# Performance work log

Measured on AMD Instinct MI355X. Metric: run time of the kernel, lower is better.

The kernel has to match this reference:

```python
import jax, jax.numpy as jnp
import numpy as np

NUM_EXPERTS = 8
AUX_LOSS_COEF = 0.01


def setup_inputs() -> dict:
    key = jax.random.key(0)
    ks = jax.random.split(key, 5)
    B, S, D, E, H = 4, 2048, 1024, NUM_EXPERTS, 4096
    scale = 0.02  # typical init scale so gelu/softmax stay in sane ranges
    return {
        "hidden_states": jax.random.normal(ks[0], (B, S, D), dtype=jnp.float32),
        "router_w": jax.random.normal(ks[1], (D, E), dtype=jnp.float32) * scale,
        "router_b": jnp.zeros((E,), dtype=jnp.float32),
        "w1": jax.random.normal(ks[2], (E, D, H), dtype=jnp.float32) * scale,
        "b1": jnp.zeros((E, H), dtype=jnp.float32),
        "w2": jax.random.normal(ks[3], (E, H, D), dtype=jnp.float32) * scale,
        "b2": jnp.zeros((E, D), dtype=jnp.float32),
    }


def reference(hidden_states, router_w, router_b, w1, b1, w2, b2):
    B, S, D = hidden_states.shape
    E = w1.shape[0]
    x = hidden_states.reshape(-1, D)  # [T, D] flattened tokens

    # Switch router: top-1 expert, combine weight = softmax prob of chosen expert
    logits = x @ router_w + router_b                      # [T, E]
    probs = jax.nn.softmax(logits, axis=-1)               # [T, E]
    sel = jnp.argmax(logits, axis=-1)                     # [T] int
    gate = jnp.take_along_axis(probs, sel[:, None], axis=1)[:, 0]  # [T]

    # Expert FFNs: per-expert Linear -> gelu -> Linear, masked top-1 combine.
    # Loop is over the small fixed expert count (structurally distinct weights).
    out = jnp.zeros_like(x)
    for e in range(E):
        h = jax.nn.gelu(x @ w1[e] + b1[e])                # [T, H]
        ye = h @ w2[e] + b2[e]                            # [T, D]
        mask = (sel == e).astype(x.dtype)
        out = out + (mask * gate)[:, None] * ye

    # Switch load-balancing auxiliary loss
    mean_probs = probs.mean(axis=0)                       # [E]
    assignments = jnp.mean(jax.nn.one_hot(sel, E, dtype=x.dtype), axis=0)  # [E]
    aux_loss = jnp.sum(mean_probs * assignments) * E
    total_loss = AUX_LOSS_COEF * aux_loss

    return out.reshape(B, S, D), total_loss
```

## Files before the change

### kernel.cpp

```cpp
#include <hip/hip_runtime.h>
#include <cstdint>

typedef __bf16 bf16_t;
typedef __attribute__((ext_vector_type(8))) __bf16 bf16x8;
typedef __attribute__((ext_vector_type(4))) float f32x4;
typedef unsigned short ushort_t;

#define TOKENS 8192
#define DIM 1024
#define HID 4096
#define NEXP 8


__device__ __forceinline__ void gl_lds16(const void* g, void* l) {
  __builtin_amdgcn_global_load_lds(
      (__attribute__((address_space(1))) void*)(void*)g,
      (__attribute__((address_space(3))) void*)l, 16, 0, 0);
}

__device__ __forceinline__ float gelu_fast(float x) {
  float x2 = x * x;
  float z2 = x * (1.59576912f + 0.07135482f * x2);
  float e = __expf(-z2);
  return x * __builtin_amdgcn_rcpf(1.f + e);
}

template <int N>
__device__ __forceinline__ void pwait() {
  __builtin_amdgcn_sched_barrier(0);
  if constexpr (N == 8) asm volatile("s_waitcnt vmcnt(8)" ::: "memory");
  else if constexpr (N == 4) asm volatile("s_waitcnt vmcnt(4)" ::: "memory");
  else asm volatile("s_waitcnt vmcnt(0)" ::: "memory");
  __builtin_amdgcn_sched_barrier(0);
  __builtin_amdgcn_s_barrier();
  __builtin_amdgcn_sched_barrier(0);
}

__device__ __forceinline__ int xcd_chunk(int f, int nwg) {
  int q = nwg >> 3, r = nwg & 7;
  int xcd = f & 7, pos = f >> 3;
  return (xcd < r) ? (xcd * (q + 1) + pos) : (r * (q + 1) + (xcd - r) * q + pos);
}

__global__ void prep_kernel(const float* __restrict__ w1, bf16_t* __restrict__ w1t,
                            const float* __restrict__ x, const float* __restrict__ rw,
                            const float* __restrict__ rbias, bf16_t* __restrict__ xb,
                            int* __restrict__ sel, float* __restrict__ gate,
                            float* __restrict__ pprob, int* __restrict__ pcnt) {
  int bid = blockIdx.x;
  int t = threadIdx.x;
  if (bid < 8192) {
    __shared__ float tile[64][65];
    int e = bid >> 10, xb_ = bid & 1023;
    const float* src = w1 + (size_t)e * DIM * HID;
    bf16_t* dst = w1t + (size_t)e * DIM * HID;
    int rt = xb_ >> 6, ct = xb_ & 63;
    int rb = rt * 64, cb = ct * 64;
    int r = t >> 2, cq = (t & 3) * 16;
    const float* sp = src + (size_t)(rb + r) * HID + cb + cq;
#pragma unroll
    for (int j = 0; j < 16; j += 4) {
      float4 v = *(const float4*)(sp + j);
      tile[r][cq + j + 0] = v.x; tile[r][cq + j + 1] = v.y;
      tile[r][cq + j + 2] = v.z; tile[r][cq + j + 3] = v.w;
    }
    __syncthreads();
    int oc = t >> 2, orr = (t & 3) * 16;
    ushort_t tmp[16];
#pragma unroll
    for (int j = 0; j < 16; ++j) {
      bf16_t b = (bf16_t)tile[orr + j][oc];
      tmp[j] = __builtin_bit_cast(ushort_t, b);
    }
    uint4* dp = (uint4*)(dst + (size_t)(cb + oc) * DIM + rb + orr);
    dp[0] = ((uint4*)tmp)[0];
    dp[1] = ((uint4*)tmp)[1];
  } else {
    __shared__ float sprob[NEXP];
    __shared__ int scnt[NEXP];
    int rblk = bid - 8192;
    int lane = t & 63, wave = t >> 6;
    if (t < NEXP) { sprob[t] = 0.f; scnt[t] = 0; }
    __syncthreads();
    int tok = rblk * 4 + wave;
    const float* xp = x + (size_t)tok * DIM + lane * 16;
    float acc[NEXP];
#pragma unroll
    for (int e = 0; e < NEXP; ++e) acc[e] = 0.f;
    ushort_t xv[16];
#pragma unroll
    for (int j = 0; j < 16; j += 4) {
      float4 v = *(const float4*)(xp + j);
      const float* wr = rw + (size_t)(lane * 16 + j) * NEXP;
      float c[4] = {v.x, v.y, v.z, v.w};
#pragma unroll
      for (int d = 0; d < 4; ++d) {
        xv[j + d] = __builtin_bit_cast(ushort_t, (bf16_t)c[d]);
#pragma unroll
        for (int e = 0; e < NEXP; ++e) acc[e] += c[d] * wr[d * NEXP + e];
      }
    }
    {
      uint4* xop = (uint4*)(xb + (size_t)tok * DIM + lane * 16);
      xop[0] = ((uint4*)xv)[0];
      xop[1] = ((uint4*)xv)[1];
    }
#pragma unroll
    for (int s = 1; s < 64; s <<= 1)
#pragma unroll
      for (int e = 0; e < NEXP; ++e) acc[e] += __shfl_xor(acc[e], s);
    if (lane == 0) {
      float lg[NEXP];
#pragma unroll
      for (int e = 0; e < NEXP; ++e) lg[e] = acc[e] + rbias[e];
      float mx = lg[0]; int am = 0;
#pragma unroll
      for (int e = 1; e < NEXP; ++e) if (lg[e] > mx) { mx = lg[e]; am = e; }
      float p[NEXP]; float se = 0.f;
#pragma unroll
      for (int e = 0; e < NEXP; ++e) { p[e] = __expf(lg[e] - mx); se += p[e]; }
      float inv = 1.f / se;
#pragma unroll
      for (int e = 0; e < NEXP; ++e) { p[e] *= inv; atomicAdd(&sprob[e], p[e]); }
      sel[tok] = am;
      gate[tok] = p[am];
      atomicAdd(&scnt[am], 1);
    }
    __syncthreads();
    if (t < NEXP) {
      pprob[rblk * NEXP + t] = sprob[t];
      pcnt[rblk * NEXP + t] = scnt[t];
    }
  }
}

__global__ void reduce_kernel(const float* __restrict__ pprob, const int* __restrict__ pcnt,
                              int nb, int* __restrict__ meta, float* __restrict__ loss_out) {
  __shared__ float fred[256];
  __shared__ int ired[256];
  int t = threadIdx.x;
  int e = t & 7, i0 = t >> 3;
  float fs = 0.f; int is = 0;
  for (int i = i0; i < nb; i += 32) { fs += pprob[i * 8 + e]; is += pcnt[i * 8 + e]; }
  fred[t] = fs; ired[t] = is;
  __syncthreads();
  if (t < NEXP) {
    float tp = 0.f; int tc = 0;
    for (int j = 0; j < 32; ++j) { tp += fred[j * 8 + t]; tc += ired[j * 8 + t]; }
    meta[t] = tc;
    fred[t] = tp;
    meta[16 + t] = 0;
  }
  __syncthreads();
  if (t == 0) {
    int off = 0; float loss = 0.f; int s1 = 0, s2 = 0;
    for (int q = 0; q < NEXP; ++q) {
      int c = meta[q];
      meta[8 + q] = off;
      int nt1 = (c + 255) >> 8;
      for (int m = 0; m < nt1; ++m) meta[32 + s1++] = (q << 16) | m;
      int nt2 = (c + 127) >> 7;
      for (int m = 0; m < nt2; ++m) meta[96 + s2++] = (q << 16) | m;
      off += c;
      loss += (fred[q] / (float)TOKENS) * ((float)c / (float)TOKENS);
    }
    meta[24] = s1;
    meta[25] = s2;
    *loss_out = loss * (float)NEXP * 0.01f;
  }
}

__global__ void scatter_kernel(const int* __restrict__ sel, int* __restrict__ meta,
                               int* __restrict__ idxl) {
  int tok = blockIdx.x * 256 + threadIdx.x;
  int lane = threadIdx.x & 63;
  int e = sel[tok];
  const int* offsets = meta + 8;
  int* cursors = meta + 16;
#pragma unroll
  for (int ex = 0; ex < NEXP; ++ex) {
    unsigned long long mask = __ballot(e == ex);
    if (e == ex) {
      int leader = __ffsll(mask) - 1;
      int total = __popcll(mask);
      int rank = __popcll(mask & ((1ull << lane) - 1ull));
      int base = 0;
      if (lane == leader) base = atomicAdd(&cursors[ex], total);
      base = __shfl(base, leader);
      idxl[offsets[ex] + base + rank] = tok;
    }
  }
}

#define STG(Q, KT) do {                                                      \
    int _kb = (KT) * 32;                                                     \
    gl_lds16(apA0 + _kb, L + (Q) * 16384 + wave * 512);                      \
    gl_lds16(apA1 + _kb, L + (Q) * 16384 + 4096 + wave * 512);               \
    gl_lds16(bpB0 + _kb, L + (Q) * 16384 + 8192 + wave * 512);               \
    gl_lds16(bpB1 + _kb, L + (Q) * 16384 + 12288 + wave * 512);              \
  } while (0)

#define CMP(Q) do {                                                          \
    const bf16_t* Ab = L + (Q) * 16384;                                      \
    const bf16_t* Bb = Ab + 8192;                                            \
    bf16x8 bv[4];                                                            \
    _Pragma("unroll")                                                        \
    for (int n = 0; n < 4; ++n)                                              \
      bv[n] = *(const bf16x8*)&Bb[(wcol * 64 + n * 16 + l15) * 32 + ks];     \
    __builtin_amdgcn_s_setprio(1);                                           \
    _Pragma("unroll")                                                        \
    for (int m = 0; m < 8; ++m) {                                            \
      bf16x8 af = *(const bf16x8*)&Ab[(wrow * 128 + m * 16 + l15) * 32 + ks];\
      _Pragma("unroll")                                                      \
      for (int n = 0; n < 4; ++n)                                            \
        acc[m][n] = __builtin_amdgcn_mfma_f32_16x16x32_bf16(af, bv[n], acc[m][n], 0, 0, 0); \
    }                                                                        \
    __builtin_amdgcn_s_setprio(0);                                           \
  } while (0)

#define PIPE(NT) do {                                                        \
    STG(0, 0); STG(1, 1); STG(2, 2);                                         \
    pwait<8>();                                                              \
    _Pragma("unroll 1")                                                      \
    for (int kt = 0; kt < (NT) - 4; kt += 4) {                               \
      STG(3, kt + 3); CMP(0); pwait<8>();                                    \
      STG(0, kt + 4); CMP(1); pwait<8>();                                    \
      STG(1, kt + 5); CMP(2); pwait<8>();                                    \
      STG(2, kt + 6); CMP(3); pwait<8>();                                    \
    }                                                                        \
    STG(3, (NT) - 1); CMP(0); pwait<8>();                                    \
    CMP(1); pwait<4>();                                                      \
    CMP(2); pwait<0>();                                                      \
    CMP(3);                                                                  \
  } while (0)

#define G1_NWG 640
#define W2_NBLK 4096

__global__ __launch_bounds__(512, 2) void gemm1_kernel(
    const bf16_t* __restrict__ xb, const bf16_t* __restrict__ w1t,
    const float* __restrict__ b1, const int* __restrict__ idxl,
    const int* __restrict__ meta, bf16_t* __restrict__ h,
    const float* __restrict__ w2, bf16_t* __restrict__ w2t) {
  __shared__ __align__(16) char smemraw[131072];
  int f = blockIdx.x;
  int t = threadIdx.x;

  if (f >= G1_NWG) {
    float (*tile)[65] = (float(*)[65])smemraw;
    int tb = f - G1_NWG;
    int e = tb >> 9, xb_ = tb & 511;
    const float* src = w2 + (size_t)e * HID * DIM;
    bf16_t* dst = w2t + (size_t)e * HID * DIM;
    int rt = xb_ >> 4, ct = xb_ & 15;
    int rb = rt * 128, cb = ct * 64;
    int r = t >> 2, cq = (t & 3) * 16;
    const float* sp = src + (size_t)(rb + r) * DIM + cb + cq;
#pragma unroll
    for (int j = 0; j < 16; j += 4) {
      float4 v = *(const float4*)(sp + j);
      tile[r][cq + j + 0] = v.x; tile[r][cq + j + 1] = v.y;
      tile[r][cq + j + 2] = v.z; tile[r][cq + j + 3] = v.w;
    }
    __syncthreads();
    int oc = t >> 3, orr = (t & 7) * 16;
    ushort_t tmp[16];
#pragma unroll
    for (int j = 0; j < 16; ++j) {
      bf16_t b = (bf16_t)tile[orr + j][oc];
      tmp[j] = __builtin_bit_cast(ushort_t, b);
    }
    uint4* dp = (uint4*)(dst + (size_t)(cb + oc) * HID + rb + orr);
    dp[0] = ((uint4*)tmp)[0];
    dp[1] = ((uint4*)tmp)[1];
    return;
  }

  bf16_t* L = (bf16_t*)smemraw;
  int lf = xcd_chunk(f, G1_NWG);
  int slot = lf % 40, nt = lf / 40;
  if (slot >= meta[24]) return;
  int tm = meta[32 + slot];
  int e = tm >> 16, mt = tm & 0xffff;
  int cnt = meta[e];
  int off = meta[8 + e];
  int mBase = mt * 256;
  int nBase = nt * 256;
  int lane = t & 63, wave = t >> 6;
  int l15 = lane & 15, g = lane >> 4;
  int wrow = wave >> 2, wcol = wave & 3;
  int ks = (g ^ (l15 & 3)) * 8;
  f32x4 acc[8][4];
#pragma unroll
  for (int m = 0; m < 8; ++m)
#pragma unroll
    for (int n = 0; n < 4; ++n) acc[m][n] = (f32x4){0.f, 0.f, 0.f, 0.f};

  int srow = t >> 2;
  int koff = ((t & 3) ^ (srow & 3)) * 8;
  int c1 = cnt - 1;
  int sA0 = mBase + srow; sA0 = sA0 < c1 ? sA0 : c1;
  int sA1 = mBase + 128 + srow; sA1 = sA1 < c1 ? sA1 : c1;
  const bf16_t* apA0 = xb + (size_t)idxl[off + sA0] * DIM + koff;
  const bf16_t* apA1 = xb + (size_t)idxl[off + sA1] * DIM + koff;
  const bf16_t* wb = w1t + (size_t)e * HID * DIM;
  const bf16_t* bpB0 = wb + (size_t)(nBase + srow) * DIM + koff;
  const bf16_t* bpB1 = wb + (size_t)(nBase + 128 + srow) * DIM + koff;

  PIPE(32);

  float bias[4];
#pragma unroll
  for (int n = 0; n < 4; ++n) bias[n] = b1[e * HID + nBase + wcol * 64 + n * 16 + l15];
#pragma unroll
  for (int m = 0; m < 8; ++m) {
    int rb0 = mBase + wrow * 128 + m * 16 + g * 4;
#pragma unroll
    for (int j = 0; j < 4; ++j) {
      int r = rb0 + j;
      if (r < cnt) {
        bf16_t* hp = h + (size_t)(off + r) * HID + nBase + wcol * 64 + l15;
#pragma unroll
        for (int n = 0; n < 4; ++n)
          hp[n * 16] = (bf16_t)gelu_fast(acc[m][n][j] + bias[n]);
      }
    }
  }
}

__global__ __launch_bounds__(512, 2) void gemm2_kernel(
    const bf16_t* __restrict__ h, const bf16_t* __restrict__ w2t,
    const float* __restrict__ b2, const int* __restrict__ idxl,
    const float* __restrict__ gate, const int* __restrict__ meta,
    float* __restrict__ out) {
  __shared__ bf16_t L[65536];
  int S = gridDim.x;
  int f = blockIdx.y * S + blockIdx.x;
  int lf = xcd_chunk(f, S * gridDim.y);
  int slot = lf % S, nt = lf / S;
  if (slot >= meta[24]) return;
  int tm = meta[32 + slot];
  int e = tm >> 16, mt = tm & 0xffff;
  int cnt = meta[e];
  int off = meta[8 + e];
  int mBase = mt * 256;
  int nBase = nt * 256;
  int t = threadIdx.x, lane = t & 63, wave = t >> 6;
  int l15 = lane & 15, g = lane >> 4;
  int wrow = wave >> 2, wcol = wave & 3;
  int ks = (g ^ (l15 & 3)) * 8;
  f32x4 acc[8][4];
#pragma unroll
  for (int m = 0; m < 8; ++m)
#pragma unroll
    for (int n = 0; n < 4; ++n) acc[m][n] = (f32x4){0.f, 0.f, 0.f, 0.f};

  int srow = t >> 2;
  int koff = ((t & 3) ^ (srow & 3)) * 8;
  int c1 = cnt - 1;
  int sA0 = mBase + srow; sA0 = sA0 < c1 ? sA0 : c1;
  int sA1 = mBase + 128 + srow; sA1 = sA1 < c1 ? sA1 : c1;
  const bf16_t* apA0 = h + (size_t)(off + sA0) * HID + koff;
  const bf16_t* apA1 = h + (size_t)(off + sA1) * HID + koff;
  const bf16_t* wb = w2t + (size_t)e * DIM * HID;
  const bf16_t* bpB0 = wb + (size_t)(nBase + srow) * HID + koff;
  const bf16_t* bpB1 = wb + (size_t)(nBase + 128 + srow) * HID + koff;

  PIPE(128);

  float bias[4];
#pragma unroll
  for (int n = 0; n < 4; ++n) bias[n] = b2[e * DIM + nBase + wcol * 64 + n * 16 + l15];
#pragma unroll
  for (int m = 0; m < 8; ++m) {
    int rb0 = mBase + wrow * 128 + m * 16 + g * 4;
#pragma unroll
    for (int j = 0; j < 4; ++j) {
      int r = rb0 + j;
      if (r < cnt) {
        int tok = idxl[off + r];
        float gg = gate[tok];
        float* op = out + (size_t)tok * DIM + nBase + wcol * 64 + l15;
#pragma unroll
        for (int n = 0; n < 4; ++n)
          op[n * 16] = gg * (acc[m][n][j] + bias[n]);
      }
    }
  }
}

extern "C" void kernel_launch(void* const* d_in, const int* in_sizes, int n_in,
                              void* d_out, int out_size, void* d_ws, size_t ws_size,
                              hipStream_t stream) {
  const float* hs = (const float*)d_in[0];
  const float* rw = (const float*)d_in[1];
  const float* rb = (const float*)d_in[2];
  const float* w1 = (const float*)d_in[3];
  const float* b1 = (const float*)d_in[4];
  const float* w2 = (const float*)d_in[5];
  const float* b2 = (const float*)d_in[6];
  float* out = (float*)d_out;
  char* ws = (char*)d_ws;

  bf16_t* xb   = (bf16_t*)(ws + 0);
  bf16_t* w1t  = (bf16_t*)(ws + 16777216);
  bf16_t* w2t  = (bf16_t*)(ws + 83886080);
  bf16_t* hbuf = (bf16_t*)(ws + 150994944);
  int*   sel   = (int*)  (ws + 220200960);
  float* gate  = (float*)(ws + 220233728);
  int*   idxl  = (int*)  (ws + 220266496);
  float* pprob = (float*)(ws + 220299264);
  int*   pcnt  = (int*)  (ws + 220364800);
  int*   meta  = (int*)  (ws + 220430336);

  prep_kernel<<<10240, 256, 0, stream>>>(w1, w1t, hs, rw, rb, xb,
                                         sel, gate, pprob, pcnt);
  reduce_kernel<<<1, 256, 0, stream>>>(pprob, pcnt, 2048, meta, out + (out_size - 1));
  scatter_kernel<<<32, 256, 0, stream>>>(sel, meta, idxl);
  gemm1_kernel<<<G1_NWG + W2_NBLK, 512, 0, stream>>>(xb, w1t, b1, idxl, meta, hbuf,
                                                     w2, w2t);
  gemm2_kernel<<<dim3(40, 4), 512, 0, stream>>>(hbuf, w2t, b2, idxl, gate, meta, out);
}
```

Measured before the change: 361.4 us.

## Halve gemm2 N-tile to 128 and enlarge prep blocks to 512 threads

gemm2 now uses 256x128 output tiles, with a 4x2 wave layout, three loads per stage, a smaller LDS ring and adjusted waitcnt depths, over a grid twice as large (40x8). The aim is more workgroups for better CU occupancy and load balance on the skewed per-expert M. The cost is less B-tile reuse per A load, so h is re-read more often. Separately, prep_kernel moves to 512-thread blocks that transpose 128x64 tiles and route 8 tokens per block, halving the grid, and the reduce count is updated to match.

```diff
diff --git a/kernel.cpp b/kernel.cpp
--- a/kernel.cpp
+++ b/kernel.cpp
@@ -29,7 +29,9 @@
 __device__ __forceinline__ void pwait() {
   __builtin_amdgcn_sched_barrier(0);
   if constexpr (N == 8) asm volatile("s_waitcnt vmcnt(8)" ::: "memory");
+  else if constexpr (N == 6) asm volatile("s_waitcnt vmcnt(6)" ::: "memory");
   else if constexpr (N == 4) asm volatile("s_waitcnt vmcnt(4)" ::: "memory");
+  else if constexpr (N == 3) asm volatile("s_waitcnt vmcnt(3)" ::: "memory");
   else asm volatile("s_waitcnt vmcnt(0)" ::: "memory");
   __builtin_amdgcn_sched_barrier(0);
   __builtin_amdgcn_s_barrier();
@@ -42,20 +44,21 @@
   return (xcd < r) ? (xcd * (q + 1) + pos) : (r * (q + 1) + (xcd - r) * q + pos);
 }
 
-__global__ void prep_kernel(const float* __restrict__ w1, bf16_t* __restrict__ w1t,
-                            const float* __restrict__ x, const float* __restrict__ rw,
-                            const float* __restrict__ rbias, bf16_t* __restrict__ xb,
-                            int* __restrict__ sel, float* __restrict__ gate,
-                            float* __restrict__ pprob, int* __restrict__ pcnt) {
+__global__ __launch_bounds__(512) void prep_kernel(
+    const float* __restrict__ w1, bf16_t* __restrict__ w1t,
+    const float* __restrict__ x, const float* __restrict__ rw,
+    const float* __restrict__ rbias, bf16_t* __restrict__ xb,
+    int* __restrict__ sel, float* __restrict__ gate,
+    float* __restrict__ pprob, int* __restrict__ pcnt) {
   int bid = blockIdx.x;
   int t = threadIdx.x;
-  if (bid < 8192) {
-    __shared__ float tile[64][65];
-    int e = bid >> 10, xb_ = bid & 1023;
+  if (bid < 4096) {
+    __shared__ float tile[128][65];
+    int e = bid >> 9, xb_ = bid & 511;
     const float* src = w1 + (size_t)e * DIM * HID;
     bf16_t* dst = w1t + (size_t)e * DIM * HID;
     int rt = xb_ >> 6, ct = xb_ & 63;
-    int rb = rt * 64, cb = ct * 64;
+    int rb = rt * 128, cb = ct * 64;
     int r = t >> 2, cq = (t & 3) * 16;
     const float* sp = src + (size_t)(rb + r) * HID + cb + cq;
 #pragma unroll
@@ -65,7 +68,7 @@
       tile[r][cq + j + 2] = v.z; tile[r][cq + j + 3] = v.w;
     }
     __syncthreads();
-    int oc = t >> 2, orr = (t & 3) * 16;
+    int oc = t >> 3, orr = (t & 7) * 16;
     ushort_t tmp[16];
 #pragma unroll
     for (int j = 0; j < 16; ++j) {
@@ -78,11 +81,11 @@
   } else {
     __shared__ float sprob[NEXP];
     __shared__ int scnt[NEXP];
-    int rblk = bid - 8192;
+    int rblk = bid - 4096;
     int lane = t & 63, wave = t >> 6;
     if (t < NEXP) { sprob[t] = 0.f; scnt[t] = 0; }
     __syncthreads();
-    int tok = rblk * 4 + wave;
+    int tok = rblk * 8 + wave;
     const float* xp = x + (size_t)tok * DIM + lane * 16;
     float acc[NEXP];
 #pragma unroll
@@ -192,7 +195,7 @@
   }
 }
 
-#define STG(Q, KT) do {                                                      \
+#define STG1(Q, KT) do {                                                     \
     int _kb = (KT) * 32;                                                     \
     gl_lds16(apA0 + _kb, L + (Q) * 16384 + wave * 512);                      \
     gl_lds16(apA1 + _kb, L + (Q) * 16384 + 4096 + wave * 512);               \
@@ -200,7 +203,7 @@
     gl_lds16(bpB1 + _kb, L + (Q) * 16384 + 12288 + wave * 512);              \
   } while (0)
 
-#define CMP(Q) do {                                                          \
+#define CMP1(Q) do {                                                         \
     const bf16_t* Ab = L + (Q) * 16384;                                      \
     const bf16_t* Bb = Ab + 8192;                                            \
     bf16x8 bv[4];                                                            \
@@ -218,20 +221,20 @@
     __builtin_amdgcn_s_setprio(0);                                           \
   } while (0)
 
-#define PIPE(NT) do {                                                        \
-    STG(0, 0); STG(1, 1); STG(2, 2);                                         \
+#define PIPE1(NT) do {                                                       \
+    STG1(0, 0); STG1(1, 1); STG1(2, 2);                                      \
     pwait<8>();                                                              \
     _Pragma("unroll 1")                                                      \
     for (int kt = 0; kt < (NT) - 4; kt += 4) {                               \
-      STG(3, kt + 3); CMP(0); pwait<8>();                                    \
-      STG(0, kt + 4); CMP(1); pwait<8>();                                    \
-      STG(1, kt + 5); CMP(2); pwait<8>();                                    \
-      STG(2, kt + 6); CMP(3); pwait<8>();                                    \
+      STG1(3, kt + 3); CMP1(0); pwait<8>();                                  \
+      STG1(0, kt + 4); CMP1(1); pwait<8>();                                  \
+      STG1(1, kt + 5); CMP1(2); pwait<8>();                                  \
+      STG1(2, kt + 6); CMP1(3); pwait<8>();                                  \
     }                                                                        \
-    STG(3, (NT) - 1); CMP(0); pwait<8>();                                    \
-    CMP(1); pwait<4>();                                                      \
-    CMP(2); pwait<0>();                                                      \
-    CMP(3);                                                                  \
+    STG1(3, (NT) - 1); CMP1(0); pwait<8>();                                  \
+    CMP1(1); pwait<4>();                                                     \
+    CMP1(2); pwait<0>();                                                     \
+    CMP1(3);                                                                 \
   } while (0)
 
 #define G1_NWG 640
@@ -307,7 +310,7 @@
   const bf16_t* bpB0 = wb + (size_t)(nBase + srow) * DIM + koff;
   const bf16_t* bpB1 = wb + (size_t)(nBase + 128 + srow) * DIM + koff;
 
-  PIPE(32);
+  PIPE1(32);
 
   float bias[4];
 #pragma unroll
@@ -327,13 +330,55 @@
     }
   }
 }
+
+#define STG2(Q, KT) do {                                                     \
+    int _kb = (KT) * 32;                                                     \
+    gl_lds16(apA0 + _kb, L + (Q) * 12288 + wave * 512);                      \
+    gl_lds16(apA1 + _kb, L + (Q) * 12288 + 4096 + wave * 512);               \
+    gl_lds16(bpB0 + _kb, L + (Q) * 12288 + 8192 + wave * 512);               \
+  } while (0)
+
+#define CMP2(Q) do {                                                         \
+    const bf16_t* Ab = L + (Q) * 12288;                                      \
+    const bf16_t* Bb = Ab + 8192;                                            \
+    bf16x8 af[4], bv[4];                                                     \
+    _Pragma("unroll")                                                        \
+    for (int m = 0; m < 4; ++m)                                              \
+      af[m] = *(const bf16x8*)&Ab[(wrow * 64 + m * 16 + l15) * 32 + ks];     \
+    _Pragma("unroll")                                                        \
+    for (int n = 0; n < 4; ++n)                                              \
+      bv[n] = *(const bf16x8*)&Bb[(wcol * 64 + n * 16 + l15) * 32 + ks];     \
+    __builtin_amdgcn_s_setprio(1);                                           \
+    _Pragma("unroll")                                                        \
+    for (int m = 0; m < 4; ++m)                                              \
+      _Pragma("unroll")                                                      \
+      for (int n = 0; n < 4; ++n)                                            \
+        acc[m][n] = __builtin_amdgcn_mfma_f32_16x16x32_bf16(af[m], bv[n], acc[m][n], 0, 0, 0); \
+    __builtin_amdgcn_s_setprio(0);                                           \
+  } while (0)
+
+#define PIPE2(NT) do {                                                       \
+    STG2(0, 0); STG2(1, 1); STG2(2, 2);                                      \
+    pwait<6>();                                                              \
+    _Pragma("unroll 1")                                                      \
+    for (int kt = 0; kt < (NT) - 4; kt += 4) {                               \
+      STG2(3, kt + 3); CMP2(0); pwait<6>();                                  \
+      STG2(0, kt + 4); CMP2(1); pwait<6>();                                  \
+      STG2(1, kt + 5); CMP2(2); pwait<6>();                                  \
+      STG2(2, kt + 6); CMP2(3); pwait<6>();                                  \
+    }                                                                        \
+    STG2(3, (NT) - 1); CMP2(0); pwait<6>();                                  \
+    CMP2(1); pwait<3>();                                                     \
+    CMP2(2); pwait<0>();                                                     \
+    CMP2(3);                                                                 \
+  } while (0)
 
 __global__ __launch_bounds__(512, 2) void gemm2_kernel(
     const bf16_t* __restrict__ h, const bf16_t* __restrict__ w2t,
     const float* __restrict__ b2, const int* __restrict__ idxl,
     const float* __restrict__ gate, const int* __restrict__ meta,
     float* __restrict__ out) {
-  __shared__ bf16_t L[65536];
+  __shared__ bf16_t L[49152];
   int S = gridDim.x;
   int f = blockIdx.y * S + blockIdx.x;
   int lf = xcd_chunk(f, S * gridDim.y);
@@ -344,14 +389,14 @@
   int cnt = meta[e];
   int off = meta[8 + e];
   int mBase = mt * 256;
-  int nBase = nt * 256;
+  int nBase = nt * 128;
   int t = threadIdx.x, lane = t & 63, wave = t >> 6;
   int l15 = lane & 15, g = lane >> 4;
-  int wrow = wave >> 2, wcol = wave & 3;
+  int wrow = wave >> 1, wcol = wave & 1;
   int ks = (g ^ (l15 & 3)) * 8;
-  f32x4 acc[8][4];
-#pragma unroll
-  for (int m = 0; m < 8; ++m)
+  f32x4 acc[4][4];
+#pragma unroll
+  for (int m = 0; m < 4; ++m)
 #pragma unroll
     for (int n = 0; n < 4; ++n) acc[m][n] = (f32x4){0.f, 0.f, 0.f, 0.f};
 
@@ -364,16 +409,15 @@
   const bf16_t* apA1 = h + (size_t)(off + sA1) * HID + koff;
   const bf16_t* wb = w2t + (size_t)e * DIM * HID;
   const bf16_t* bpB0 = wb + (size_t)(nBase + srow) * HID + koff;
-  const bf16_t* bpB1 = wb + (size_t)(nBase + 128 + srow) * HID + koff;
-
-  PIPE(128);
+
+  PIPE2(128);
 
   float bias[4];
 #pragma unroll
   for (int n = 0; n < 4; ++n) bias[n] = b2[e * DIM + nBase + wcol * 64 + n * 16 + l15];
 #pragma unroll
-  for (int m = 0; m < 8; ++m) {
-    int rb0 = mBase + wrow * 128 + m * 16 + g * 4;
+  for (int m = 0; m < 4; ++m) {
+    int rb0 = mBase + wrow * 64 + m * 16 + g * 4;
 #pragma unroll
     for (int j = 0; j < 4; ++j) {
       int r = rb0 + j;
@@ -413,11 +457,11 @@
   int*   pcnt  = (int*)  (ws + 220364800);
   int*   meta  = (int*)  (ws + 220430336);
 
-  prep_kernel<<<10240, 256, 0, stream>>>(w1, w1t, hs, rw, rb, xb,
-                                         sel, gate, pprob, pcnt);
-  reduce_kernel<<<1, 256, 0, stream>>>(pprob, pcnt, 2048, meta, out + (out_size - 1));
+  prep_kernel<<<5120, 512, 0, stream>>>(w1, w1t, hs, rw, rb, xb,
+                                        sel, gate, pprob, pcnt);
+  reduce_kernel<<<1, 256, 0, stream>>>(pprob, pcnt, 1024, meta, out + (out_size - 1));
   scatter_kernel<<<32, 256, 0, stream>>>(sel, meta, idxl);
   gemm1_kernel<<<G1_NWG + W2_NBLK, 512, 0, stream>>>(xb, w1t, b1, idxl, meta, hbuf,
                                                      w2, w2t);
-  gemm2_kernel<<<dim3(40, 4), 512, 0, stream>>>(hbuf, w2t, b2, idxl, gate, meta, out);
-}
+  gemm2_kernel<<<dim3(40, 8), 512, 0, stream>>>(hbuf, w2t, b2, idxl, gate, meta, out);
+}
```

Result: slower. 371.3 us (+2.8%).
